# Optimization experiments

Hardware: AMD Instinct MI355X
Metric: run time of the kernel (lower is better)

Reference implementation:

```python
import jax, jax.numpy as jnp
import numpy as np

N = 100000   # nodes (in_ch)
D = 128      # emb_ch
E = 1600000  # nonzeros in A_hat
RATE = 0.1   # dropout rate


def setup_inputs() -> dict:
    key = jax.random.key(0)
    k1, k2, k3, k4, k5, k6 = jax.random.split(key, 6)
    x = jnp.arange(N, dtype=jnp.int64) if jax.config.jax_enable_x64 else jnp.arange(N, dtype=jnp.int32)
    rows = jax.random.randint(k1, (E,), 0, N)
    cols = jax.random.randint(k2, (E,), 0, N)
    A_vals = jax.random.uniform(k3, (E,), dtype=jnp.float32)
    # xavier_uniform for [N, D]: bound = sqrt(6/(N+D))
    bound = float(np.sqrt(6.0 / (N + D)))
    emb_weight = jax.random.uniform(k4, (N, D), jnp.float32, -bound, bound)
    u1 = jax.random.uniform(k5, (N, D), dtype=jnp.float32)
    u2 = jax.random.uniform(k6, (N, D), dtype=jnp.float32)
    return {"x": x, "rows": rows, "cols": cols, "A_vals": A_vals,
            "emb_weight": emb_weight, "u1": u1, "u2": u2}


def _dropout(h, u):
    keep = (u >= RATE).astype(h.dtype)
    return h * keep / (1.0 - RATE)


def _spmm(rows, cols, vals, h):
    # out[i] = sum_{e: rows[e]==i} vals[e] * h[cols[e]]  -- COO SpMM
    msgs = vals[:, None] * h[cols]  # [E, D]
    return jax.ops.segment_sum(msgs, rows, num_segments=N)


def reference(x, rows, cols, A_vals, emb_weight, u1, u2):
    h0 = emb_weight[x]                       # embedding lookup [N, D]
    h1 = _spmm(rows, cols, A_vals, _dropout(h0, u1))
    h2 = _spmm(rows, cols, A_vals, _dropout(h1, u2))
    return (h0 + h1 + h2) / 3.0
```

## Files before the change

kernel.cpp:

```cpp
#include <hip/hip_runtime.h>
#include <hip/hip_fp16.h>

#define DD 128
#define SCAN_CHUNK 1024
#define ROWS_PER_BLK 16
#define MAX_STAGE 512
#define NCOPY 8

typedef float          f32x4 __attribute__((ext_vector_type(4)));
typedef unsigned int   u32x4 __attribute__((ext_vector_type(4)));
typedef unsigned int   u32x2 __attribute__((ext_vector_type(2)));
typedef unsigned short u16x8 __attribute__((ext_vector_type(8)));

struct __align__(8) Edge { int c; float v; };

__device__ __forceinline__ unsigned short f2h(float f) {
    return __half_as_ushort(__float2half(f));
}
__device__ __forceinline__ float2 up2(unsigned int u) {
    __half2 h = *reinterpret_cast<const __half2*>(&u);
    return __half22float2(h);
}

template <typename T>
__device__ __forceinline__ T ldnt(const T* p) { return __builtin_nontemporal_load(p); }
template <typename T>
__device__ __forceinline__ void stnt(T* p, T v) { __builtin_nontemporal_store(v, p); }

__global__ __launch_bounds__(256) void k_g1hist(const float* __restrict__ emb,
                                                const float* __restrict__ u1,
                                                ushort* __restrict__ g1,
                                                const int* __restrict__ rows,
                                                int* __restrict__ cnt8,
                                                ushort* __restrict__ rank,
                                                int total8, int E, int N) {
    int i = blockIdx.x * 256 + threadIdx.x;
    bool doE = i < E;
    bool doS = i < total8;
    int r = 0;
    if (doE) r = ldnt(rows + i);
    f32x4 hA, hB, uA, uB;
    if (doS) {
        const f32x4* e4 = (const f32x4*)emb;
        const f32x4* a4 = (const f32x4*)u1;
        hA = ldnt(e4 + 2 * (size_t)i);
        hB = ldnt(e4 + 2 * (size_t)i + 1);
        uA = ldnt(a4 + 2 * (size_t)i);
        uB = ldnt(a4 + 2 * (size_t)i + 1);
    }
    if (doE) {
        int k = blockIdx.x & (NCOPY - 1);
        int old = atomicAdd(&cnt8[(size_t)k * N + r], 1);
        stnt(rank + i, (ushort)((k << 13) | old));
    }
    if (doS) {
        const float s = 1.0f / 0.9f;
        u16x8 g;
        g[0] = f2h((uA.x >= 0.1f) ? hA.x * s : 0.0f);
        g[1] = f2h((uA.y >= 0.1f) ? hA.y * s : 0.0f);
        g[2] = f2h((uA.z >= 0.1f) ? hA.z * s : 0.0f);
        g[3] = f2h((uA.w >= 0.1f) ? hA.w * s : 0.0f);
        g[4] = f2h((uB.x >= 0.1f) ? hB.x * s : 0.0f);
        g[5] = f2h((uB.y >= 0.1f) ? hB.y * s : 0.0f);
        g[6] = f2h((uB.z >= 0.1f) ? hB.z * s : 0.0f);
        g[7] = f2h((uB.w >= 0.1f) ? hB.w * s : 0.0f);
        ((u16x8*)g1)[i] = g;
    }
}

__global__ __launch_bounds__(256) void k_scan1(int* __restrict__ cnt8,
                                               int* __restrict__ rs,
                                               int* __restrict__ bsum, int n) {
    __shared__ int s[256];
    int tid = threadIdx.x;
    int base = blockIdx.x * SCAN_CHUNK + tid * 4;
    int tot[4];
#pragma unroll
    for (int j = 0; j < 4; ++j) {
        int row = base + j;
        int t = 0;
        if (row < n) {
            int c[NCOPY];
#pragma unroll
            for (int k = 0; k < NCOPY; ++k) c[k] = cnt8[(size_t)k * n + row];
#pragma unroll
            for (int k = 0; k < NCOPY; ++k) {
                int cc = c[k];
                cnt8[(size_t)k * n + row] = t;
                t += cc;
            }
        }
        tot[j] = t;
    }
    int tsum = tot[0] + tot[1] + tot[2] + tot[3];
    s[tid] = tsum;
    __syncthreads();
    for (int off = 1; off < 256; off <<= 1) {
        int t = (tid >= off) ? s[tid - off] : 0;
        __syncthreads();
        s[tid] += t;
        __syncthreads();
    }
    int excl = s[tid] - tsum;
    if (tid == 255) bsum[blockIdx.x] = s[255];
    int run = excl;
#pragma unroll
    for (int j = 0; j < 4; ++j) {
        int row = base + j;
        if (row < n) rs[row] = run;
        run += tot[j];
    }
}

__global__ __launch_bounds__(256) void k_scan23(int* __restrict__ rs,
                                                const int* __restrict__ bsum,
                                                int nb, int n) {
    __shared__ int s[1024];
    int tid = threadIdx.x;
    for (int i = tid; i < nb; i += 256) s[i] = bsum[i];
    __syncthreads();
    if (tid == 0) {
        int run = 0;
        for (int i = 0; i < nb; ++i) { int t = s[i]; s[i] = run; run += t; }
    }
    __syncthreads();
    int i = blockIdx.x * 256 + tid;
    if (i < n) rs[i] += s[i >> 10];
}

__global__ __launch_bounds__(256) void k_scatter_prep(const int* __restrict__ rows,
                                                      const int* __restrict__ cols,
                                                      const float* __restrict__ vals,
                                                      const int* __restrict__ rs,
                                                      const int* __restrict__ cnt8,
                                                      const ushort* __restrict__ rank,
                                                      Edge* __restrict__ ev,
                                                      const float* __restrict__ emb,
                                                      const float* __restrict__ u2,
                                                      ushort* __restrict__ emb16,
                                                      unsigned char* __restrict__ mask2,
                                                      int E, int total8, int N) {
    int i = blockIdx.x * 256 + threadIdx.x;
    bool doE = i < E;
    bool doS = i < total8;
    int r = 0, c = 0; float v = 0.f; unsigned int rk = 0;
    if (doE) {
        r = ldnt(rows + i);
        c = ldnt(cols + i);
        v = ldnt(vals + i);
        rk = ldnt(rank + i);
    }
    f32x4 hA, hB, vA, vB;
    if (doS) {
        const f32x4* e4 = (const f32x4*)emb;
        const f32x4* b4 = (const f32x4*)u2;
        hA = ldnt(e4 + 2 * (size_t)i);
        hB = ldnt(e4 + 2 * (size_t)i + 1);
        vA = ldnt(b4 + 2 * (size_t)i);
        vB = ldnt(b4 + 2 * (size_t)i + 1);
    }
    if (doE) {
        int k = rk >> 13;
        int rin = rk & 0x1FFF;
        int pos = rs[r] + cnt8[(size_t)k * N + r] + rin;
        u32x2 q;
        q.x = (unsigned int)c;
        q.y = __float_as_uint(v);
        ((u32x2*)ev)[pos] = q;
    }
    if (doS) {
        u16x8 e16;
        e16[0] = f2h(hA.x); e16[1] = f2h(hA.y); e16[2] = f2h(hA.z); e16[3] = f2h(hA.w);
        e16[4] = f2h(hB.x); e16[5] = f2h(hB.y); e16[6] = f2h(hB.z); e16[7] = f2h(hB.w);
        stnt((u16x8*)emb16 + i, e16);
        unsigned char m =
            (unsigned char)((vA.x >= 0.1f ? 1u : 0u)  | (vA.y >= 0.1f ? 2u : 0u)  |
                            (vA.z >= 0.1f ? 4u : 0u)  | (vA.w >= 0.1f ? 8u : 0u)  |
                            (vB.x >= 0.1f ? 16u : 0u) | (vB.y >= 0.1f ? 32u : 0u) |
                            (vB.z >= 0.1f ? 64u : 0u) | (vB.w >= 0.1f ? 128u : 0u));
        stnt(mask2 + i, m);
    }
}

template <int MODE>
__global__ __launch_bounds__(256) void k_gather(const int* __restrict__ rowstart,
                                                const Edge* __restrict__ ev,
                                                const ushort* __restrict__ srch,
                                                const unsigned char* __restrict__ mask2,
                                                const ushort* __restrict__ emb16,
                                                const ushort* __restrict__ p16in,
                                                ushort* __restrict__ p16out,
                                                ushort* __restrict__ g2,
                                                float* __restrict__ out,
                                                int N, int E) {
    __shared__ int s_rs[ROWS_PER_BLK + 1];
    __shared__ Edge s_ev[MAX_STAGE];

    int tid = threadIdx.x;
    int r0 = blockIdx.x * ROWS_PER_BLK;
    if (tid <= ROWS_PER_BLK) {
        int r = r0 + tid;
        s_rs[tid] = (r < N) ? rowstart[r] : E;
    }
    __syncthreads();
    int base = s_rs[0];
    int nblk = s_rs[ROWS_PER_BLK] - base;
    int nstage = nblk < MAX_STAGE ? nblk : MAX_STAGE;
    for (int i = tid; i < nstage; i += 256) {
        u32x2 q = ldnt((const u32x2*)(ev + base + i));
        Edge ed; ed.c = (int)q.x; ed.v = __uint_as_float(q.y);
        s_ev[i] = ed;
    }
    __syncthreads();

    int grp = tid >> 4;
    int lane = tid & 15;
    int row = r0 + grp;
    if (row >= N) return;
    int start = s_rs[grp] - base;
    int end = s_rs[grp + 1] - base;
    int eL = end < nstage ? end : nstage;

    const u32x4* __restrict__ s4 = (const u32x4*)srch;
    const Edge* __restrict__ evg = ev + base;
    float a0 = 0.f, a1 = 0.f, a2 = 0.f, a3 = 0.f;
    float a4 = 0.f, a5 = 0.f, a6 = 0.f, a7 = 0.f;

#define LDE(i) Edge E##i = s_ev[e + i];
#define GQ(i)  u32x4 q##i = s4[((size_t)E##i.c << 4) + lane];
#define ACC(i) { float vv = E##i.v; \
        float2 w0 = up2(q##i.x), w1 = up2(q##i.y), w2 = up2(q##i.z), w3 = up2(q##i.w); \
        a0 = fmaf(vv, w0.x, a0); a1 = fmaf(vv, w0.y, a1); \
        a2 = fmaf(vv, w1.x, a2); a3 = fmaf(vv, w1.y, a3); \
        a4 = fmaf(vv, w2.x, a4); a5 = fmaf(vv, w2.y, a5); \
        a6 = fmaf(vv, w3.x, a6); a7 = fmaf(vv, w3.y, a7); }

    int e = start;
    for (; e + 8 <= eL; e += 8) {
        LDE(0) LDE(1) LDE(2) LDE(3) LDE(4) LDE(5) LDE(6) LDE(7)
        GQ(0) GQ(1) GQ(2) GQ(3) GQ(4) GQ(5) GQ(6) GQ(7)
        ACC(0) ACC(1) ACC(2) ACC(3) ACC(4) ACC(5) ACC(6) ACC(7)
    }
    if (e + 4 <= eL) {
        LDE(0) LDE(1) LDE(2) LDE(3)
        GQ(0) GQ(1) GQ(2) GQ(3)
        ACC(0) ACC(1) ACC(2) ACC(3)
        e += 4;
    }
    for (; e < eL; ++e) {
        LDE(0) GQ(0) ACC(0)
    }
    for (; e < end; ++e) {
        Edge E0; { u32x2 q_ = ldnt((const u32x2*)(evg + e));
                   E0.c = (int)q_.x; E0.v = __uint_as_float(q_.y); }
        GQ(0) ACC(0)
    }
#undef LDE
#undef GQ
#undef ACC

    size_t o = ((size_t)row << 7) + (size_t)lane * 8;
    if (MODE == 1) {
        unsigned int m = ldnt(mask2 + (size_t)row * 16 + lane);
        const float s = 1.0f / 0.9f;
        u16x8 gg;
        gg[0] = (m & 1u)   ? f2h(a0 * s) : (ushort)0;
        gg[1] = (m & 2u)   ? f2h(a1 * s) : (ushort)0;
        gg[2] = (m & 4u)   ? f2h(a2 * s) : (ushort)0;
        gg[3] = (m & 8u)   ? f2h(a3 * s) : (ushort)0;
        gg[4] = (m & 16u)  ? f2h(a4 * s) : (ushort)0;
        gg[5] = (m & 32u)  ? f2h(a5 * s) : (ushort)0;
        gg[6] = (m & 64u)  ? f2h(a6 * s) : (ushort)0;
        gg[7] = (m & 128u) ? f2h(a7 * s) : (ushort)0;
        stnt((u16x8*)(g2 + o), gg);
        u16x8 pp;
        pp[0] = f2h(a0); pp[1] = f2h(a1); pp[2] = f2h(a2); pp[3] = f2h(a3);
        pp[4] = f2h(a4); pp[5] = f2h(a5); pp[6] = f2h(a6); pp[7] = f2h(a7);
        stnt((u16x8*)(p16out + o), pp);
    } else {
        u32x4 eq = ldnt((const u32x4*)(emb16 + o));
        u32x4 pq = ldnt((const u32x4*)(p16in + o));
        float2 e0 = up2(eq.x), e1 = up2(eq.y), e2 = up2(eq.z), e3 = up2(eq.w);
        float2 p0 = up2(pq.x), p1 = up2(pq.y), p2 = up2(pq.z), p3 = up2(pq.w);
        const float t3 = 1.0f / 3.0f;
        f32x4 rA, rB;
        rA.x = (e0.x + p0.x + a0) * t3;
        rA.y = (e0.y + p0.y + a1) * t3;
        rA.z = (e1.x + p1.x + a2) * t3;
        rA.w = (e1.y + p1.y + a3) * t3;
        rB.x = (e2.x + p2.x + a4) * t3;
        rB.y = (e2.y + p2.y + a5) * t3;
        rB.z = (e3.x + p3.x + a6) * t3;
        rB.w = (e3.y + p3.y + a7) * t3;
        stnt((f32x4*)(out + o), rA);
        stnt((f32x4*)(out + o) + 1, rB);
    }
}


extern "C" void kernel_launch(void* const* d_in, const int* in_sizes, int n_in,
                              void* d_out, int out_size, void* d_ws, size_t ws_size,
                              hipStream_t stream) {
    const int* rows = (const int*)d_in[1];
    const int* cols = (const int*)d_in[2];
    const float* vals = (const float*)d_in[3];
    const float* emb = (const float*)d_in[4];
    const float* u1 = (const float*)d_in[5];
    const float* u2 = (const float*)d_in[6];
    float* out = (float*)d_out;

    const int N = in_sizes[0];
    const int E = in_sizes[1];
    const size_t ND = (size_t)N * DD;

    char* ws = (char*)d_ws;
    Edge* ev     = (Edge*)ws;   ws += (size_t)E * sizeof(Edge);
    ushort* g1   = (ushort*)ws; ws += ND * sizeof(ushort);
    ushort* g2   = (ushort*)ws; ws += ND * sizeof(ushort);
    ushort* p16  = (ushort*)ws; ws += ND * sizeof(ushort);
    ushort* emb16= (ushort*)ws; ws += ND * sizeof(ushort);
    int* cnt8    = (int*)ws;    ws += (size_t)NCOPY * N * sizeof(int);
    int* rs      = (int*)ws;    ws += (size_t)N * sizeof(int);
    ushort* rank = (ushort*)ws; ws += (size_t)E * sizeof(ushort);
    int* bsum    = (int*)ws;    ws += 4096;
    unsigned char* mask2 = (unsigned char*)ws;

    const int total8 = (int)(ND / 8);
    const int prepBlocks = (total8 + 255) / 256;
    const int gridE = (E + 255) / 256;
    const int gridFuse = prepBlocks > gridE ? prepBlocks : gridE;
    const int nScanBlocks = (N + SCAN_CHUNK - 1) / SCAN_CHUNK;
    const int gridRow = (N + ROWS_PER_BLK - 1) / ROWS_PER_BLK;

    hipMemsetAsync(cnt8, 0, (size_t)NCOPY * N * sizeof(int), stream);
    k_g1hist<<<gridFuse, 256, 0, stream>>>(emb, u1, g1, rows, cnt8, rank,
                                           total8, E, N);
    k_scan1<<<nScanBlocks, 256, 0, stream>>>(cnt8, rs, bsum, N);
    k_scan23<<<(N + 255) / 256, 256, 0, stream>>>(rs, bsum, nScanBlocks, N);
    k_scatter_prep<<<gridFuse, 256, 0, stream>>>(rows, cols, vals, rs, cnt8, rank,
                                                 ev, emb, u2, emb16, mask2,
                                                 E, total8, N);
    k_gather<1><<<gridRow, 256, 0, stream>>>(rs, ev, g1, mask2, nullptr, nullptr,
                                             p16, g2, nullptr, N, E);
    k_gather<2><<<gridRow, 256, 0, stream>>>(rs, ev, g2, nullptr, emb16, p16,
                                             nullptr, nullptr, out, N, E);
}
```

Baseline: 419.1 us.

## Split gather across column halves, batch edges per thread, fold offsets into cnt8

The gather kernels now use a 2D grid. Each block handles 32 rows over one 64-column half, with 8 lanes per row and a larger shared edge stage. The histogram and scatter kernels process 4 edges per thread, so edge blocks shrink to a quarter of their former count and sit alongside the elementwise prep work. The scan now writes absolute per-copy offsets into cnt8, so the scatter no longer reads rs. This is meant to raise gather parallelism and cut scatter lookups, at the cost of staging each row's edge list twice and extra cnt8 writes in the scans.

New measurement: 425.7 us. No clear change (+1.6%).

```diff
diff --git a/kernel.cpp b/kernel.cpp
--- a/kernel.cpp
+++ b/kernel.cpp
@@ -3,8 +3,8 @@
 
 #define DD 128
 #define SCAN_CHUNK 1024
-#define ROWS_PER_BLK 16
-#define MAX_STAGE 512
+#define G_ROWS 32
+#define G_STAGE 1024
 #define NCOPY 8
 
 typedef float          f32x4 __attribute__((ext_vector_type(4)));
@@ -34,11 +34,20 @@
                                                 int* __restrict__ cnt8,
                                                 ushort* __restrict__ rank,
                                                 int total8, int E, int N) {
-    int i = blockIdx.x * 256 + threadIdx.x;
-    bool doE = i < E;
+    int t = threadIdx.x;
+    int b = blockIdx.x;
+    int i = b * 256 + t;
+    int e0 = b * 1024 + t;
+    int k = b & (NCOPY - 1);
     bool doS = i < total8;
-    int r = 0;
-    if (doE) r = ldnt(rows + i);
+
+    int r[4]; bool v[4];
+#pragma unroll
+    for (int j = 0; j < 4; ++j) {
+        int e = e0 + j * 256;
+        v[j] = e < E;
+        r[j] = v[j] ? ldnt(rows + e) : 0;
+    }
     f32x4 hA, hB, uA, uB;
     if (doS) {
         const f32x4* e4 = (const f32x4*)emb;
@@ -48,11 +57,14 @@
         uA = ldnt(a4 + 2 * (size_t)i);
         uB = ldnt(a4 + 2 * (size_t)i + 1);
     }
-    if (doE) {
-        int k = blockIdx.x & (NCOPY - 1);
-        int old = atomicAdd(&cnt8[(size_t)k * N + r], 1);
-        stnt(rank + i, (ushort)((k << 13) | old));
-    }
+    int old[4];
+#pragma unroll
+    for (int j = 0; j < 4; ++j)
+        if (v[j]) old[j] = atomicAdd(&cnt8[(size_t)k * N + r[j]], 1);
+#pragma unroll
+    for (int j = 0; j < 4; ++j)
+        if (v[j]) stnt(rank + e0 + j * 256, (ushort)((k << 13) | old[j]));
+
     if (doS) {
         const float s = 1.0f / 0.9f;
         u16x8 g;
@@ -74,20 +86,17 @@
     __shared__ int s[256];
     int tid = threadIdx.x;
     int base = blockIdx.x * SCAN_CHUNK + tid * 4;
+    int c[4][NCOPY];
     int tot[4];
 #pragma unroll
     for (int j = 0; j < 4; ++j) {
         int row = base + j;
         int t = 0;
         if (row < n) {
-            int c[NCOPY];
-#pragma unroll
-            for (int k = 0; k < NCOPY; ++k) c[k] = cnt8[(size_t)k * n + row];
 #pragma unroll
             for (int k = 0; k < NCOPY; ++k) {
-                int cc = c[k];
-                cnt8[(size_t)k * n + row] = t;
-                t += cc;
+                c[j][k] = cnt8[(size_t)k * n + row];
+                t += c[j][k];
             }
         }
         tot[j] = t;
@@ -107,12 +116,21 @@
 #pragma unroll
     for (int j = 0; j < 4; ++j) {
         int row = base + j;
-        if (row < n) rs[row] = run;
+        if (row < n) {
+            rs[row] = run;
+            int p = run;
+#pragma unroll
+            for (int k = 0; k < NCOPY; ++k) {
+                cnt8[(size_t)k * n + row] = p;
+                p += c[j][k];
+            }
+        }
         run += tot[j];
     }
 }
 
 __global__ __launch_bounds__(256) void k_scan23(int* __restrict__ rs,
+                                                int* __restrict__ cnt8,
                                                 const int* __restrict__ bsum,
                                                 int nb, int n) {
     __shared__ int s[1024];
@@ -125,13 +143,17 @@
     }
     __syncthreads();
     int i = blockIdx.x * 256 + tid;
-    if (i < n) rs[i] += s[i >> 10];
+    if (i < n) {
+        int off = s[i >> 10];
+        rs[i] += off;
+#pragma unroll
+        for (int k = 0; k < NCOPY; ++k) cnt8[(size_t)k * n + i] += off;
+    }
 }
 
 __global__ __launch_bounds__(256) void k_scatter_prep(const int* __restrict__ rows,
                                                       const int* __restrict__ cols,
                                                       const float* __restrict__ vals,
-                                                      const int* __restrict__ rs,
                                                       const int* __restrict__ cnt8,
                                                       const ushort* __restrict__ rank,
                                                       Edge* __restrict__ ev,
@@ -140,15 +162,23 @@
                                                       ushort* __restrict__ emb16,
                                                       unsigned char* __restrict__ mask2,
                                                       int E, int total8, int N) {
-    int i = blockIdx.x * 256 + threadIdx.x;
-    bool doE = i < E;
+    int t = threadIdx.x;
+    int b = blockIdx.x;
+    int i = b * 256 + t;
+    int e0 = b * 1024 + t;
     bool doS = i < total8;
-    int r = 0, c = 0; float v = 0.f; unsigned int rk = 0;
-    if (doE) {
-        r = ldnt(rows + i);
-        c = ldnt(cols + i);
-        v = ldnt(vals + i);
-        rk = ldnt(rank + i);
+
+    int r[4], c[4]; float vv[4]; unsigned int rk[4]; bool v[4];
+#pragma unroll
+    for (int j = 0; j < 4; ++j) {
+        int e = e0 + j * 256;
+        v[j] = e < E;
+        if (v[j]) {
+            r[j] = ldnt(rows + e);
+            c[j] = ldnt(cols + e);
+            vv[j] = ldnt(vals + e);
+            rk[j] = ldnt(rank + e);
+        }
     }
     f32x4 hA, hB, vA, vB;
     if (doS) {
@@ -159,14 +189,17 @@
         vA = ldnt(b4 + 2 * (size_t)i);
         vB = ldnt(b4 + 2 * (size_t)i + 1);
     }
-    if (doE) {
-        int k = rk >> 13;
-        int rin = rk & 0x1FFF;
-        int pos = rs[r] + cnt8[(size_t)k * N + r] + rin;
-        u32x2 q;
-        q.x = (unsigned int)c;
-        q.y = __float_as_uint(v);
-        ((u32x2*)ev)[pos] = q;
+#pragma unroll
+    for (int j = 0; j < 4; ++j) {
+        if (v[j]) {
+            int kk = rk[j] >> 13;
+            int rin = rk[j] & 0x1FFF;
+            int pos = cnt8[(size_t)kk * N + r[j]] + rin;
+            u32x2 q;
+            q.x = (unsigned int)c[j];
+            q.y = __float_as_uint(vv[j]);
+            ((u32x2*)ev)[pos] = q;
+        }
     }
     if (doS) {
         u16x8 e16;
@@ -193,19 +226,20 @@
                                                 ushort* __restrict__ g2,
                                                 float* __restrict__ out,
                                                 int N, int E) {
-    __shared__ int s_rs[ROWS_PER_BLK + 1];
-    __shared__ Edge s_ev[MAX_STAGE];
+    __shared__ int s_rs[G_ROWS + 1];
+    __shared__ Edge s_ev[G_STAGE];
 
     int tid = threadIdx.x;
-    int r0 = blockIdx.x * ROWS_PER_BLK;
-    if (tid <= ROWS_PER_BLK) {
+    int r0 = blockIdx.x * G_ROWS;
+    int h = blockIdx.y;
+    if (tid <= G_ROWS) {
         int r = r0 + tid;
         s_rs[tid] = (r < N) ? rowstart[r] : E;
     }
     __syncthreads();
     int base = s_rs[0];
-    int nblk = s_rs[ROWS_PER_BLK] - base;
-    int nstage = nblk < MAX_STAGE ? nblk : MAX_STAGE;
+    int nblk = s_rs[G_ROWS] - base;
+    int nstage = nblk < G_STAGE ? nblk : G_STAGE;
     for (int i = tid; i < nstage; i += 256) {
         u32x2 q = ldnt((const u32x2*)(ev + base + i));
         Edge ed; ed.c = (int)q.x; ed.v = __uint_as_float(q.y);
@@ -213,8 +247,8 @@
     }
     __syncthreads();
 
-    int grp = tid >> 4;
-    int lane = tid & 15;
+    int grp = tid >> 3;
+    int lane = tid & 7;
     int row = r0 + grp;
     if (row >= N) return;
     int start = s_rs[grp] - base;
@@ -223,11 +257,12 @@
 
     const u32x4* __restrict__ s4 = (const u32x4*)srch;
     const Edge* __restrict__ evg = ev + base;
+    int hoff = (h << 3) + lane;
     float a0 = 0.f, a1 = 0.f, a2 = 0.f, a3 = 0.f;
     float a4 = 0.f, a5 = 0.f, a6 = 0.f, a7 = 0.f;
 
 #define LDE(i) Edge E##i = s_ev[e + i];
-#define GQ(i)  u32x4 q##i = s4[((size_t)E##i.c << 4) + lane];
+#define GQ(i)  u32x4 q##i = s4[((size_t)E##i.c << 4) + hoff];
 #define ACC(i) { float vv = E##i.v; \
         float2 w0 = up2(q##i.x), w1 = up2(q##i.y), w2 = up2(q##i.z), w3 = up2(q##i.w); \
         a0 = fmaf(vv, w0.x, a0); a1 = fmaf(vv, w0.y, a1); \
@@ -259,9 +294,9 @@
 #undef GQ
 #undef ACC
 
-    size_t o = ((size_t)row << 7) + (size_t)lane * 8;
+    size_t o = ((size_t)row << 7) + ((size_t)h << 6) + (size_t)lane * 8;
     if (MODE == 1) {
-        unsigned int m = ldnt(mask2 + (size_t)row * 16 + lane);
+        unsigned int m = mask2[(size_t)row * 16 + (h << 3) + lane];
         const float s = 1.0f / 0.9f;
         u16x8 gg;
         gg[0] = (m & 1u)   ? f2h(a0 * s) : (ushort)0;
@@ -327,17 +362,18 @@
 
     const int total8 = (int)(ND / 8);
     const int prepBlocks = (total8 + 255) / 256;
-    const int gridE = (E + 255) / 256;
+    const int gridE = (E + 1023) / 1024;
     const int gridFuse = prepBlocks > gridE ? prepBlocks : gridE;
     const int nScanBlocks = (N + SCAN_CHUNK - 1) / SCAN_CHUNK;
-    const int gridRow = (N + ROWS_PER_BLK - 1) / ROWS_PER_BLK;
+    const int gridRowX = (N + G_ROWS - 1) / G_ROWS;
+    dim3 gridRow(gridRowX, 2, 1);
 
     hipMemsetAsync(cnt8, 0, (size_t)NCOPY * N * sizeof(int), stream);
     k_g1hist<<<gridFuse, 256, 0, stream>>>(emb, u1, g1, rows, cnt8, rank,
                                            total8, E, N);
     k_scan1<<<nScanBlocks, 256, 0, stream>>>(cnt8, rs, bsum, N);
-    k_scan23<<<(N + 255) / 256, 256, 0, stream>>>(rs, bsum, nScanBlocks, N);
-    k_scatter_prep<<<gridFuse, 256, 0, stream>>>(rows, cols, vals, rs, cnt8, rank,
+    k_scan23<<<(N + 255) / 256, 256, 0, stream>>>(rs, cnt8, bsum, nScanBlocks, N);
+    k_scatter_prep<<<gridFuse, 256, 0, stream>>>(rows, cols, vals, cnt8, rank,
                                                  ev, emb, u2, emb16, mask2,
                                                  E, total8, N);
     k_gather<1><<<gridRow, 256, 0, stream>>>(rs, ev, g1, mask2, nullptr, nullptr,
```
